# Performance work log

Hardware: AMD Instinct MI355X
Metric: run time of the kernel (lower is better)

Reference implementation:

```python
import jax, jax.numpy as jnp
import numpy as np

Dm = 512      # d_model
DI = 1024     # d_inner = 2*d_model (expand=2)
DR = 32       # dt_rank = ceil(d_model/16)
DC = 4        # d_conv
T = 3
Bb, Sf, H, W = 2, 15, 16, 11


def _ln(x, g, b):
    m = jnp.mean(x, axis=-1, keepdims=True)
    v = jnp.var(x, axis=-1, keepdims=True)
    return (x - m) * jax.lax.rsqrt(v + 1e-5) * g + b


def _mamba(x, in_w, conv_w, conv_b, xproj_w, dtproj_w, dtproj_b, A_log, D_param, out_w):
    # x: (B, L, Dm). Standard Mamba block with d_state=1.
    B, L, _ = x.shape
    xz = x @ in_w.T                                  # (B, L, 2*DI)
    xi, z = jnp.split(xz, 2, axis=-1)                # each (B, L, DI)
    # causal depthwise conv1d, kernel DC
    xc = jnp.transpose(xi, (0, 2, 1))                # (B, DI, L)
    xc = jax.lax.conv_general_dilated(
        xc, conv_w[:, None, :], (1,), [(DC - 1, 0)],
        dimension_numbers=('NCH', 'OIH', 'NCH'), feature_group_count=DI)
    xc = xc + conv_b[None, :, None]
    xi = jax.nn.silu(jnp.transpose(xc, (0, 2, 1)))   # (B, L, DI)
    x_dbl = xi @ xproj_w.T                           # (B, L, DR + 2)  (d_state=1)
    dt = x_dbl[..., :DR]
    Bc = x_dbl[..., DR:DR + 1]                       # (B, L, 1)
    Cc = x_dbl[..., DR + 1:DR + 2]                   # (B, L, 1)
    dt = jax.nn.softplus(dt @ dtproj_w.T + dtproj_b)  # (B, L, DI)
    A = -jnp.exp(A_log[:, 0])                        # (DI,), d_state=1
    dA = jnp.exp(dt * A)                             # (B, L, DI)
    dBx = dt * Bc * xi                               # (B, L, DI)
    # linear recurrence h_t = dA_t * h_{t-1} + dBx_t via parallel scan
    def comb(l, r):
        return (l[0] * r[0], r[0] * l[1] + r[1])
    _, h = jax.lax.associative_scan(comb, (dA, dBx), axis=1)
    y = Cc * h + D_param * xi                        # (B, L, DI)
    y = y * jax.nn.silu(z)
    return y @ out_w.T                               # (B, L, Dm)


def setup_inputs() -> dict:
    key = jax.random.key(0)
    ks = jax.random.split(key, 10)
    p = {}
    p['x'] = jax.random.normal(ks[0], (Bb, Sf, H, W, Dm), jnp.float32)
    p['ln1_g'] = jnp.ones((Dm,), jnp.float32)
    p['ln1_b'] = jnp.zeros((Dm,), jnp.float32)
    p['ln2_g'] = jnp.ones((Dm,), jnp.float32)
    p['ln2_b'] = jnp.zeros((Dm,), jnp.float32)
    p['mlp_w1'] = jax.random.normal(ks[1], (4 * Dm, Dm), jnp.float32) * 0.02
    p['mlp_b1'] = jnp.zeros((4 * Dm,), jnp.float32)
    p['mlp_w2'] = jax.random.normal(ks[2], (Dm, 4 * Dm), jnp.float32) * 0.02
    p['mlp_b2'] = jnp.zeros((Dm,), jnp.float32)
    p['in_w'] = jax.random.normal(ks[3], (2 * DI, Dm), jnp.float32) * 0.02
    p['conv_w'] = jax.random.normal(ks[4], (DI, DC), jnp.float32) * 0.1
    p['conv_b'] = jnp.zeros((DI,), jnp.float32)
    p['xproj_w'] = jax.random.normal(ks[5], (DR + 2, DI), jnp.float32) * 0.02
    p['dtproj_w'] = jax.random.normal(ks[6], (DI, DR), jnp.float32) * 0.1
    p['dtproj_b'] = jax.random.normal(ks[7], (DI,), jnp.float32) * 0.1
    p['A_log'] = jnp.zeros((DI, 1), jnp.float32)     # A = -1 per channel (mamba init, d_state=1)
    p['D_param'] = jnp.ones((DI,), jnp.float32)
    p['out_w'] = jax.random.normal(ks[8], (Dm, DI), jnp.float32) * 0.02
    return p


def reference(x, ln1_g, ln1_b, ln2_g, ln2_b, mlp_w1, mlp_b1, mlp_w2, mlp_b2,
              in_w, conv_w, conv_b, xproj_w, dtproj_w, dtproj_b, A_log, D_param, out_w):
    b, S, h, w, c = x.shape
    s = S // T
    xr = x.reshape(b * s, T, h, w, c)
    Bm, L = b * s, T * h * w
    # ---- part1: 4-directional mamba over flattened/flipped sequences ----
    xn = _ln(xr, ln1_g, ln1_b)
    x1 = xn.reshape(Bm, L, c)                                  # b (s h w) c
    x3 = jnp.transpose(xn, (0, 1, 3, 2, 4)).reshape(Bm, L, c)  # b (s w h) c
    cat = jnp.concatenate([x1, jnp.flip(x1, 1), x3, jnp.flip(x3, 1)], axis=0)
    y = _mamba(cat, in_w, conv_w, conv_b, xproj_w, dtproj_w, dtproj_b, A_log, D_param, out_w)
    y1, y2, y3, y4 = jnp.split(y, 4, axis=0)
    x12 = (y1 + jnp.flip(y2, 1)).reshape(Bm, T, h, w, c)
    x34 = jnp.transpose((y3 + jnp.flip(y4, 1)).reshape(Bm, T, w, h, c), (0, 1, 3, 2, 4))
    xr = xr + x12 + x34   # dropout (eval) = identity
    # ---- part2: MLP ----
    hmid = jax.nn.gelu(_ln(xr, ln2_g, ln2_b) @ mlp_w1.T + mlp_b1, approximate=False)
    xr = xr + (hmid @ mlp_w2.T + mlp_b2)
    return xr.reshape(b, S, h, w, c)
```

## Files before the change

### kernel.cpp

```cpp
#include <hip/hip_runtime.h>
#include <math.h>

typedef __attribute__((ext_vector_type(8))) short short8;
typedef __attribute__((ext_vector_type(8))) __bf16 bf16x8;
typedef __attribute__((ext_vector_type(4))) float f32x4;
typedef unsigned short ushort_t;

#define DEV __device__ __forceinline__

constexpr int Dm   = 512;
constexpr int DI   = 1024;
constexpr int DR   = 32;
constexpr int Hh   = 16;
constexpr int Wd   = 11;
constexpr int Bm   = 10;
constexpr int Lq   = 528;
constexpr int NTOK = Bm * Lq;
constexpr int MBAT = 4 * Bm;
constexpr int MTOK = MBAT * Lq;
constexpr int XD_LD = 40;
constexpr int NCHK = 16;
constexpr int CHK  = Lq / NCHK;
constexpr int MPAD = 5376;

DEV ushort_t f2bf(float f) {
    unsigned u = __float_as_uint(f);
    u += 0x7fffu + ((u >> 16) & 1u);
    return (ushort_t)(u >> 16);
}
DEV float bf2f(ushort_t h) { return __uint_as_float(((unsigned)h) << 16); }

DEV bf16x8 as_bf(short8 v) { return __builtin_bit_cast(bf16x8, v); }

DEV void mfma_bf16(f32x4& d, short8 a, short8 b) {
    d = __builtin_amdgcn_mfma_f32_16x16x32_bf16(as_bf(a), as_bf(b), d, 0, 0, 0);
}

DEV void gll16(const ushort_t* g, ushort_t* l) {
    __builtin_amdgcn_global_load_lds((const __attribute__((address_space(1))) void*)g,
                                     (__attribute__((address_space(3))) void*)l,
                                     16, 0, 0);
}

DEV float fast_erf(float x) {
    const float ax = fabsf(x);
    const float t  = 1.0f / (1.0f + 0.3275911f * ax);
    const float y  = t * (0.254829592f + t * (-0.284496736f + t * (1.421413741f
                   + t * (-1.453152027f + t * 1.061405429f))));
    const float r  = 1.0f - y * __expf(-ax * ax);
    return copysignf(r, x);
}

DEV int path_tok(int p, int bi, int q) {
    int ql = (p & 1) ? (Lq - 1 - q) : q;
    int l1;
    if (p < 2) {
        l1 = ql;
    } else {
        int t   = ql / (Hh * Wd);
        int rem = ql - t * (Hh * Wd);
        int ww  = rem / Hh;
        int hh  = rem - ww * Hh;
        l1 = (t * Hh + hh) * Wd + ww;
    }
    return bi * Lq + l1;
}

__global__ void k_f2bf(const float* __restrict__ s, ushort_t* __restrict__ d, int n) {
    int i = blockIdx.x * 256 + threadIdx.x;
    if (i < n) d[i] = f2bf(s[i]);
}
__global__ void k_zero(ushort_t* __restrict__ d, int n) {
    int i = blockIdx.x * 256 + threadIdx.x;
    if (i < n) d[i] = 0;
}
__global__ void k_cwT(const float* __restrict__ cw, float* __restrict__ cwT) {
    int i = blockIdx.x * 256 + threadIdx.x;
    if (i < 4 * DI) {
        int d = i / DI, ch = i - d * DI;
        cwT[i] = cw[ch * 4 + d];
    }
}

__global__ void k_ln1(const float* __restrict__ x, const float* __restrict__ g,
                      const float* __restrict__ b, ushort_t* __restrict__ xn) {
    const int tok  = blockIdx.x;
    const int lane = threadIdx.x;
    const int c0   = lane * 8;
    const float* row = x + (size_t)tok * Dm;
    float4 v0 = *(const float4*)(row + c0);
    float4 v1 = *(const float4*)(row + c0 + 4);
    float s  = v0.x + v0.y + v0.z + v0.w + v1.x + v1.y + v1.z + v1.w;
    float ss = v0.x*v0.x + v0.y*v0.y + v0.z*v0.z + v0.w*v0.w
             + v1.x*v1.x + v1.y*v1.y + v1.z*v1.z + v1.w*v1.w;
#pragma unroll
    for (int o = 32; o >= 1; o >>= 1) { s += __shfl_xor(s, o); ss += __shfl_xor(ss, o); }
    const float mean = s * (1.0f / Dm);
    const float rstd = rsqrtf(ss * (1.0f / Dm) - mean * mean + 1e-5f);
    float4 g0 = *(const float4*)(g + c0), g1 = *(const float4*)(g + c0 + 4);
    float4 b0 = *(const float4*)(b + c0), b1 = *(const float4*)(b + c0 + 4);
    union { uint4 u; ushort_t h[8]; } pk;
    pk.h[0] = f2bf((v0.x - mean) * rstd * g0.x + b0.x);
    pk.h[1] = f2bf((v0.y - mean) * rstd * g0.y + b0.y);
    pk.h[2] = f2bf((v0.z - mean) * rstd * g0.z + b0.z);
    pk.h[3] = f2bf((v0.w - mean) * rstd * g0.w + b0.w);
    pk.h[4] = f2bf((v1.x - mean) * rstd * g1.x + b1.x);
    pk.h[5] = f2bf((v1.y - mean) * rstd * g1.y + b1.y);
    pk.h[6] = f2bf((v1.z - mean) * rstd * g1.z + b1.z);
    pk.h[7] = f2bf((v1.w - mean) * rstd * g1.w + b1.w);
    *(uint4*)(xn + (size_t)tok * Dm + c0) = pk.u;
}

template<int BM, int BN, int EPI>
__launch_bounds__(512)
__global__ void k_gemm8w(const ushort_t* __restrict__ A, const ushort_t* __restrict__ B,
                         void* __restrict__ C, int M, int K,
                         int lda, int ldb, int ldc, int nst,
                         const float* __restrict__ bias, const float* __restrict__ resid) {
    constexpr int FM = BM / 32;
    constexpr int FN = BN / 64;
    constexpr int AP = BM / 64;
    constexpr int BP = BN / 64;
    __shared__ __align__(16) ushort_t As[2][BM * 64];
    __shared__ __align__(16) ushort_t Bs[2][BN * 64];
    const int tid  = threadIdx.x;
    const int lane = tid & 63;
    const int w    = tid >> 6;
    const int wm   = w >> 2, wn = w & 3;
    const int lr   = lane & 15, lg = lane >> 4;
    const int m0   = blockIdx.x * BM, n0 = blockIdx.y * BN;

    f32x4 acc[FM][FN] = {};

    auto stage = [&](int buf, int kb) {
#pragma unroll
        for (int i = 0; i < AP; ++i) {
            const int chunk = i * 512 + tid;
            const int r    = chunk >> 3;
            const int ccol = chunk & 7;
            const int csrc = ccol ^ (r & 7);
            gll16(A + (size_t)(m0 + r) * lda + kb + csrc * 8, As[buf] + chunk * 8);
        }
#pragma unroll
        for (int i = 0; i < BP; ++i) {
            const int chunk = i * 512 + tid;
            const int r    = chunk >> 3;
            const int ccol = chunk & 7;
            const int csrc = ccol ^ (r & 7);
            gll16(B + (size_t)(n0 + r) * ldb + kb + csrc * 8, Bs[buf] + chunk * 8);
        }
    };

    auto compute = [&](int buf) {
#pragma unroll
        for (int kk = 0; kk < 2; ++kk) {
            short8 a[FM], b[FN];
#pragma unroll
            for (int mf = 0; mf < FM; ++mf) {
                const int row = wm * (BM / 2) + mf * 16 + lr;
                const int pc  = (kk * 4 + lg) ^ (row & 7);
                a[mf] = *(const short8*)(As[buf] + (size_t)row * 64 + pc * 8);
            }
#pragma unroll
            for (int nf = 0; nf < FN; ++nf) {
                const int row = wn * (BN / 4) + nf * 16 + lr;
                const int pc  = (kk * 4 + lg) ^ (row & 7);
                b[nf] = *(const short8*)(Bs[buf] + (size_t)row * 64 + pc * 8);
            }
#pragma unroll
            for (int mf = 0; mf < FM; ++mf)
#pragma unroll
                for (int nf = 0; nf < FN; ++nf)
                    mfma_bf16(acc[mf][nf], a[mf], b[nf]);
        }
    };

    stage(0, 0);
    __syncthreads();
    int cur = 0;
    for (int kb = 64; kb < K; kb += 64) {
        stage(cur ^ 1, kb);
        compute(cur);
        __syncthreads();
        cur ^= 1;
    }
    compute(cur);

#pragma unroll
    for (int mf = 0; mf < FM; ++mf)
#pragma unroll
        for (int nf = 0; nf < FN; ++nf) {
            const int gc = n0 + wn * (BN / 4) + nf * 16 + lr;
            if (gc >= nst) continue;
#pragma unroll
            for (int r = 0; r < 4; ++r) {
                const int gm = m0 + wm * (BM / 2) + mf * 16 + lg * 4 + r;
                if (gm >= M) continue;
                float v = acc[mf][nf][r];
                const size_t oi = (size_t)gm * ldc + gc;
                if constexpr (EPI == 0) {
                    ((ushort_t*)C)[oi] = f2bf(v);
                } else if constexpr (EPI == 2) {
                    v += bias[gc];
                    v = 0.5f * v * (1.0f + fast_erf(v * 0.70710678118654752f));
                    ((ushort_t*)C)[oi] = f2bf(v);
                } else if constexpr (EPI == 3) {
                    v += bias[gc] + resid[oi];
                    ((float*)C)[oi] = v;
                } else if constexpr (EPI == 4) {
                    v += resid[oi];
                    ((float*)C)[oi] = v;
                }
            }
        }
}

template<int EPI>
__launch_bounds__(256)
__global__ void k_gemm_bt(const ushort_t* __restrict__ A, const ushort_t* __restrict__ B,
                          void* __restrict__ C, int M, int N, int K,
                          int lda, int ldb, int ldc,
                          const float* __restrict__ bias) {
    constexpr int BM = 64, BN = 64, BK = 64, LDL = BK + 8;
    __shared__ __align__(16) ushort_t As[BM][LDL];
    __shared__ __align__(16) ushort_t Bs[BN][LDL];
    const int tid  = threadIdx.x;
    const int m0   = blockIdx.x * BM, n0 = blockIdx.y * BN;
    const int lane = tid & 63;
    const int wv   = tid >> 6;
    const int wm   = wv >> 1, wn = wv & 1;
    const int lr   = lane & 15, lg = lane >> 4;

    f32x4 acc[2][2] = {};

    for (int kb = 0; kb < K; kb += BK) {
#pragma unroll
        for (int j = 0; j < 2; ++j) {
            const int chunk = tid + j * 256;
            const int row = chunk >> 3;
            const int k0  = (chunk & 7) << 3;
            const int gk  = kb + k0;
            short8 va = {};
            const int gm = m0 + row;
            if (gm < M && gk < K) va = *(const short8*)(A + (size_t)gm * lda + gk);
            *(short8*)(&As[row][k0]) = va;
            short8 vb = {};
            const int gn = n0 + row;
            if (gn < N && gk < K) vb = *(const short8*)(B + (size_t)gn * ldb + gk);
            *(short8*)(&Bs[row][k0]) = vb;
        }
        __syncthreads();
#pragma unroll
        for (int kk = 0; kk < 2; ++kk) {
            short8 a0 = *(const short8*)(&As[wm * 32 +  0 + lr][kk * 32 + lg * 8]);
            short8 a1 = *(const short8*)(&As[wm * 32 + 16 + lr][kk * 32 + lg * 8]);
            short8 b0 = *(const short8*)(&Bs[wn * 32 +  0 + lr][kk * 32 + lg * 8]);
            short8 b1 = *(const short8*)(&Bs[wn * 32 + 16 + lr][kk * 32 + lg * 8]);
            mfma_bf16(acc[0][0], a0, b0);
            mfma_bf16(acc[0][1], a0, b1);
            mfma_bf16(acc[1][0], a1, b0);
            mfma_bf16(acc[1][1], a1, b1);
        }
        __syncthreads();
    }

#pragma unroll
    for (int mf = 0; mf < 2; ++mf)
#pragma unroll
        for (int nf = 0; nf < 2; ++nf) {
            const int gc = n0 + wn * 32 + nf * 16 + lr;
            if (gc >= N) continue;
#pragma unroll
            for (int r = 0; r < 4; ++r) {
                const int gm = m0 + wm * 32 + mf * 16 + lg * 4 + r;
                if (gm >= M) continue;
                float v = acc[mf][nf][r];
                const size_t oi = (size_t)gm * ldc + gc;
                if constexpr (EPI == 0) {
                    ((ushort_t*)C)[oi] = f2bf(v);
                } else {
                    v += bias[gc];
                    v = fmaxf(v, 0.0f) + __logf(1.0f + __expf(-fabsf(v)));
                    ((ushort_t*)C)[oi] = f2bf(v);
                }
            }
        }
}

__global__ void k_conv(const ushort_t* __restrict__ xz0, const float* __restrict__ cwT,
                       const float* __restrict__ cb, ushort_t* __restrict__ xi) {
    const int idx = blockIdx.x * 256 + threadIdx.x;
    if (idx >= MTOK * 128) return;
    const int g  = idx & 127;
    const int c0 = g * 8;
    const int l  = (idx >> 7) % Lq;
    const int s  = idx / (128 * Lq);
    const int p  = s / Bm, bi = s % Bm;
    float a[8];
    {
        float4 b0 = *(const float4*)(cb + c0);
        float4 b1 = *(const float4*)(cb + c0 + 4);
        a[0]=b0.x; a[1]=b0.y; a[2]=b0.z; a[3]=b0.w;
        a[4]=b1.x; a[5]=b1.y; a[6]=b1.z; a[7]=b1.w;
    }
#pragma unroll
    for (int d = 0; d < 4; ++d) {
        const int lq = l - (3 - d);
        if (lq < 0) continue;
        const int tok = path_tok(p, bi, lq);
        union U { uint4 u; ushort_t h[8]; } xv;
        xv.u = *(const uint4*)(xz0 + (size_t)tok * (2 * DI) + c0);
        const float4 w0 = *(const float4*)(cwT + d * DI + c0);
        const float4 w1 = *(const float4*)(cwT + d * DI + c0 + 4);
        a[0] += bf2f(xv.h[0]) * w0.x;
        a[1] += bf2f(xv.h[1]) * w0.y;
        a[2] += bf2f(xv.h[2]) * w0.z;
        a[3] += bf2f(xv.h[3]) * w0.w;
        a[4] += bf2f(xv.h[4]) * w1.x;
        a[5] += bf2f(xv.h[5]) * w1.y;
        a[6] += bf2f(xv.h[6]) * w1.z;
        a[7] += bf2f(xv.h[7]) * w1.w;
    }
    union U { uint4 u; ushort_t h[8]; } ov;
#pragma unroll
    for (int k = 0; k < 8; ++k) {
        const float sv = a[k] / (1.0f + __expf(-a[k]));
        ov.h[k] = f2bf(sv);
    }
    *(uint4*)(xi + (size_t)(s * Lq + l) * DI + c0) = ov.u;
}

__global__ void k_scan1(const ushort_t* __restrict__ dt, const ushort_t* __restrict__ xz0,
                        const ushort_t* __restrict__ xdbl, const float* __restrict__ A_log,
                        const float* __restrict__ Dp, ushort_t* __restrict__ xiy,
                        ushort_t* __restrict__ corr, float* __restrict__ Pb,
                        float* __restrict__ Sb) {
    const int blk = blockIdx.x;
    const int cg = blk & 15;
    const int j  = (blk >> 4) & (NCHK - 1);
    const int s  = blk >> 8;
    const int ch = (cg << 6) + threadIdx.x;
    const int p  = s / Bm, bi = s % Bm;
    const int gl0 = j * CHK;
    const float Av = -__expf(A_log[ch]);
    const float Dv = Dp[ch];
    const size_t tok0 = (size_t)s * Lq + (size_t)gl0;
    const ushort_t* pdt = dt  + tok0 * DI + ch;
    ushort_t*       pxi = xiy + tok0 * DI + ch;
    ushort_t*       pco = corr + tok0 * DI + ch;
    const ushort_t* pbc = xdbl + tok0 * XD_LD;

    float h = 0.0f, pp = 1.0f;
    float dtv = bf2f(pdt[0]);
    float xiv = bf2f(pxi[0]);
    float zv  = bf2f(xz0[(size_t)path_tok(p, bi, gl0) * (2 * DI) + DI + ch]);
    float bc  = bf2f(pbc[32]);
    float cc  = bf2f(pbc[33]);
    for (int l = 0; l < CHK; ++l) {
        float ndt = 0.f, nxi = 0.f, nz = 0.f, nbc = 0.f, ncc = 0.f;
        if (l + 1 < CHK) {
            const size_t o = (size_t)(l + 1);
            ndt = bf2f(pdt[o * DI]);
            nxi = bf2f(pxi[o * DI]);
            nz  = bf2f(xz0[(size_t)path_tok(p, bi, gl0 + l + 1) * (2 * DI) + DI + ch]);
            nbc = bf2f(pbc[o * XD_LD + 32]);
            ncc = bf2f(pbc[o * XD_LD + 33]);
        }
        const float dA = __expf(dtv * Av);
        h = dA * h + dtv * bc * xiv;
        pp *= dA;
        const float sz = zv / (1.0f + __expf(-zv));
        pxi[(size_t)l * DI] = f2bf((cc * h + Dv * xiv) * sz);
        pco[(size_t)l * DI] = f2bf(cc * pp * sz);
        dtv = ndt; xiv = nxi; zv = nz; bc = nbc; cc = ncc;
    }
    const size_t pi = (size_t)(s * NCHK + j) * DI + ch;
    Pb[pi] = pp;
    Sb[pi] = h;
}

__global__ void k_scan2(const float* __restrict__ Pb, const float* __restrict__ Sb,
                        float* __restrict__ cb) {
    const int s  = blockIdx.x >> 4;
    const int ch = ((blockIdx.x & 15) << 6) + threadIdx.x;
    float c = 0.0f;
#pragma unroll
    for (int j = 0; j < NCHK; ++j) {
        const size_t pi = (size_t)(s * NCHK + j) * DI + ch;
        cb[pi] = c;
        c = Pb[pi] * c + Sb[pi];
    }
}

__global__ void k_ysum(const ushort_t* __restrict__ y, const ushort_t* __restrict__ corr,
                       const float* __restrict__ cbuf, ushort_t* __restrict__ ys) {
    const int tok = blockIdx.x;
    const int c0  = threadIdx.x * 8;
    const int bi = tok / Lq;
    const int l1 = tok % Lq;
    const int t  = l1 / (Hh * Wd);
    const int hw = l1 % (Hh * Wd);
    const int hh = hw / Wd, ww = hw % Wd;
    const int l3 = (t * Wd + ww) * Hh + hh;
    const int q[4] = { l1, Lq - 1 - l1, l3, Lq - 1 - l3 };
    float a[8] = {};
#pragma unroll
    for (int p = 0; p < 4; ++p) {
        const int sq = p * Bm + bi;
        const size_t off = ((size_t)sq * Lq + q[p]) * DI + c0;
        union U { uint4 u; ushort_t h[8]; } yv, cv;
        yv.u = *(const uint4*)(y + off);
        cv.u = *(const uint4*)(corr + off);
        const int j = q[p] / CHK;
        const float* cp = cbuf + ((size_t)sq * NCHK + j) * DI + c0;
        float4 ca = *(const float4*)(cp);
        float4 cb2 = *(const float4*)(cp + 4);
        a[0] += bf2f(yv.h[0]) + ca.x  * bf2f(cv.h[0]);
        a[1] += bf2f(yv.h[1]) + ca.y  * bf2f(cv.h[1]);
        a[2] += bf2f(yv.h[2]) + ca.z  * bf2f(cv.h[2]);
        a[3] += bf2f(yv.h[3]) + ca.w  * bf2f(cv.h[3]);
        a[4] += bf2f(yv.h[4]) + cb2.x * bf2f(cv.h[4]);
        a[5] += bf2f(yv.h[5]) + cb2.y * bf2f(cv.h[5]);
        a[6] += bf2f(yv.h[6]) + cb2.z * bf2f(cv.h[6]);
        a[7] += bf2f(yv.h[7]) + cb2.w * bf2f(cv.h[7]);
    }
    union U { uint4 u; ushort_t h[8]; } ov;
#pragma unroll
    for (int k = 0; k < 8; ++k) ov.h[k] = f2bf(a[k]);
    *(uint4*)(ys + (size_t)tok * DI + c0) = ov.u;
}

__global__ void k_ln2(const float* __restrict__ xin, const float* __restrict__ g,
                      const float* __restrict__ b, ushort_t* __restrict__ out) {
    const int tok  = blockIdx.x;
    const int lane = threadIdx.x;
    const int c0   = lane * 8;
    const float* row = xin + (size_t)tok * Dm;
    float4 v0 = *(const float4*)(row + c0);
    float4 v1 = *(const float4*)(row + c0 + 4);
    float s  = v0.x + v0.y + v0.z + v0.w + v1.x + v1.y + v1.z + v1.w;
    float ss = v0.x*v0.x + v0.y*v0.y + v0.z*v0.z + v0.w*v0.w
             + v1.x*v1.x + v1.y*v1.y + v1.z*v1.z + v1.w*v1.w;
#pragma unroll
    for (int o = 32; o >= 1; o >>= 1) { s += __shfl_xor(s, o); ss += __shfl_xor(ss, o); }
    const float mean = s * (1.0f / Dm);
    const float rstd = rsqrtf(ss * (1.0f / Dm) - mean * mean + 1e-5f);
    float4 g0 = *(const float4*)(g + c0), g1 = *(const float4*)(g + c0 + 4);
    float4 b0 = *(const float4*)(b + c0), b1 = *(const float4*)(b + c0 + 4);
    union { uint4 u; ushort_t h[8]; } pk;
    pk.h[0] = f2bf((v0.x - mean) * rstd * g0.x + b0.x);
    pk.h[1] = f2bf((v0.y - mean) * rstd * g0.y + b0.y);
    pk.h[2] = f2bf((v0.z - mean) * rstd * g0.z + b0.z);
    pk.h[3] = f2bf((v0.w - mean) * rstd * g0.w + b0.w);
    pk.h[4] = f2bf((v1.x - mean) * rstd * g1.x + b1.x);
    pk.h[5] = f2bf((v1.y - mean) * rstd * g1.y + b1.y);
    pk.h[6] = f2bf((v1.z - mean) * rstd * g1.z + b1.z);
    pk.h[7] = f2bf((v1.w - mean) * rstd * g1.w + b1.w);
    *(uint4*)(out + (size_t)tok * Dm + c0) = pk.u;
}

constexpr size_t OFF_CAT = 0;
constexpr size_t SZ_CAT  = (size_t)MPAD * Dm * 2;
constexpr size_t OFF_XZ0 = OFF_CAT + SZ_CAT;
constexpr size_t SZ_XZ0  = (size_t)MPAD * 2 * DI * 2;
constexpr size_t OFF_XI  = OFF_XZ0 + SZ_XZ0;
constexpr size_t SZ_XI   = (size_t)MTOK * DI * 2;
constexpr size_t OFF_XD  = OFF_XI + SZ_XI;
constexpr size_t SZ_XD   = (size_t)MTOK * XD_LD * 2;
constexpr size_t OFF_DT  = OFF_XD + SZ_XD;
constexpr size_t SZ_DT   = (size_t)MTOK * DI * 2;
constexpr size_t OFF_CO  = OFF_DT + SZ_DT;
constexpr size_t SZ_CO   = (size_t)MTOK * DI * 2;
constexpr size_t SZ_PSC  = (size_t)MBAT * NCHK * DI * 4;
constexpr size_t OFF_P   = OFF_CO + SZ_CO;
constexpr size_t OFF_S   = OFF_P + SZ_PSC;
constexpr size_t OFF_C   = OFF_S + SZ_PSC;
constexpr size_t OFF_YS  = OFF_C + SZ_PSC;
constexpr size_t SZ_YS   = (size_t)MPAD * DI * 2;
constexpr size_t OFF_XR2 = OFF_YS + SZ_YS;
constexpr size_t SZ_XR2  = (size_t)NTOK * Dm * 4;
constexpr size_t OFF_XL2 = OFF_XR2 + SZ_XR2;
constexpr size_t SZ_XL2  = (size_t)MPAD * Dm * 2;
constexpr size_t OFF_HM  = OFF_XL2 + SZ_XL2;
constexpr size_t SZ_HM   = (size_t)MPAD * 4 * Dm * 2;
constexpr size_t OFF_WIN = OFF_HM + SZ_HM;
constexpr size_t OFF_WOUT= OFF_WIN  + (size_t)2 * DI * Dm * 2;
constexpr size_t OFF_W1  = OFF_WOUT + (size_t)Dm * DI * 2;
constexpr size_t OFF_W2  = OFF_W1   + (size_t)4 * Dm * Dm * 2;
constexpr size_t OFF_WXP = OFF_W2   + (size_t)Dm * 4 * Dm * 2;
constexpr size_t OFF_WDT = OFF_WXP  + (size_t)64 * DI * 2;
constexpr size_t OFF_CWT = OFF_WDT  + (size_t)DI * DR * 2;
constexpr size_t WS_NEED = OFF_CWT  + (size_t)4 * DI * 4;

extern "C" void kernel_launch(void* const* d_in, const int* in_sizes, int n_in,
                              void* d_out, int out_size, void* d_ws, size_t ws_size,
                              hipStream_t stream) {
    const float* x        = (const float*)d_in[0];
    const float* ln1_g    = (const float*)d_in[1];
    const float* ln1_b    = (const float*)d_in[2];
    const float* ln2_g    = (const float*)d_in[3];
    const float* ln2_b    = (const float*)d_in[4];
    const float* mlp_w1   = (const float*)d_in[5];
    const float* mlp_b1   = (const float*)d_in[6];
    const float* mlp_w2   = (const float*)d_in[7];
    const float* mlp_b2   = (const float*)d_in[8];
    const float* in_w     = (const float*)d_in[9];
    const float* conv_w   = (const float*)d_in[10];
    const float* conv_b   = (const float*)d_in[11];
    const float* xproj_w  = (const float*)d_in[12];
    const float* dtproj_w = (const float*)d_in[13];
    const float* dtproj_b = (const float*)d_in[14];
    const float* A_log    = (const float*)d_in[15];
    const float* D_param  = (const float*)d_in[16];
    const float* out_w    = (const float*)d_in[17];

    if (ws_size < WS_NEED) return;

    char* ws = (char*)d_ws;
    ushort_t* cat   = (ushort_t*)(ws + OFF_CAT);
    ushort_t* xz0   = (ushort_t*)(ws + OFF_XZ0);
    ushort_t* xi    = (ushort_t*)(ws + OFF_XI);
    ushort_t* xdbl  = (ushort_t*)(ws + OFF_XD);
    ushort_t* dtb   = (ushort_t*)(ws + OFF_DT);
    ushort_t* corr  = (ushort_t*)(ws + OFF_CO);
    float*    Pb    = (float*)   (ws + OFF_P);
    float*    Sb    = (float*)   (ws + OFF_S);
    float*    cb    = (float*)   (ws + OFF_C);
    ushort_t* ysum  = (ushort_t*)(ws + OFF_YS);
    float*    xr2   = (float*)   (ws + OFF_XR2);
    ushort_t* xln2  = (ushort_t*)(ws + OFF_XL2);
    ushort_t* hmid  = (ushort_t*)(ws + OFF_HM);
    ushort_t* w_in  = (ushort_t*)(ws + OFF_WIN);
    ushort_t* w_out = (ushort_t*)(ws + OFF_WOUT);
    ushort_t* w_1   = (ushort_t*)(ws + OFF_W1);
    ushort_t* w_2   = (ushort_t*)(ws + OFF_W2);
    ushort_t* w_xp  = (ushort_t*)(ws + OFF_WXP);
    ushort_t* w_dt  = (ushort_t*)(ws + OFF_WDT);
    float*    cwT   = (float*)   (ws + OFF_CWT);

    auto cvt = [&](const float* s, ushort_t* d, int n) {
        k_f2bf<<<(n + 255) / 256, 256, 0, stream>>>(s, d, n);
    };
    cvt(in_w,     w_in,  2 * DI * Dm);
    cvt(out_w,    w_out, Dm * DI);
    cvt(mlp_w1,   w_1,   4 * Dm * Dm);
    cvt(mlp_w2,   w_2,   Dm * 4 * Dm);
    k_zero<<<(64 * DI + 255) / 256, 256, 0, stream>>>(w_xp, 64 * DI);
    cvt(xproj_w,  w_xp,  (DR + 2) * DI);
    cvt(dtproj_w, w_dt,  DI * DR);
    k_cwT<<<(4 * DI + 255) / 256, 256, 0, stream>>>(conv_w, cwT);

    k_ln1<<<NTOK, 64, 0, stream>>>(x, ln1_g, ln1_b, cat);

    k_gemm8w<64, 128, 0><<<dim3(MPAD / 64, (2 * DI) / 128), 512, 0, stream>>>(
        cat, w_in, xz0, NTOK, Dm, Dm, Dm, 2 * DI, 2 * DI, nullptr, nullptr);

    k_conv<<<(MTOK * 128 + 255) / 256, 256, 0, stream>>>(xz0, cwT, conv_b, xi);

    k_gemm8w<64, 64, 0><<<dim3(MTOK / 64, 1), 512, 0, stream>>>(
        xi, w_xp, xdbl, MTOK, DI, DI, DI, XD_LD, DR + 2, nullptr, nullptr);

    k_gemm_bt<1><<<dim3(MTOK / 64, DI / 64), 256, 0, stream>>>(
        xdbl, w_dt, dtb, MTOK, DI, DR, XD_LD, DR, DI, dtproj_b);

    k_scan1<<<MBAT * NCHK * 16, 64, 0, stream>>>(dtb, xz0, xdbl, A_log, D_param,
                                                 xi, corr, Pb, Sb);
    k_scan2<<<MBAT * 16, 64, 0, stream>>>(Pb, Sb, cb);

    k_ysum<<<NTOK, 128, 0, stream>>>(xi, corr, cb, ysum);

    k_gemm8w<64, 128, 4><<<dim3(MPAD / 64, Dm / 128), 512, 0, stream>>>(
        ysum, w_out, xr2, NTOK, DI, DI, DI, Dm, Dm, nullptr, x);

    k_ln2<<<NTOK, 64, 0, stream>>>(xr2, ln2_g, ln2_b, xln2);

    k_gemm8w<64, 128, 2><<<dim3(MPAD / 64, (4 * Dm) / 128), 512, 0, stream>>>(
        xln2, w_1, hmid, NTOK, Dm, Dm, Dm, 4 * Dm, 4 * Dm, mlp_b1, nullptr);

    k_gemm8w<64, 128, 3><<<dim3(MPAD / 64, Dm / 128), 512, 0, stream>>>(
        hmid, w_2, (float*)d_out, NTOK, 4 * Dm, 4 * Dm, 4 * Dm, Dm, Dm, mlp_b2, xr2);
}
```

Measured before the change: 261.1 us.

## Move silu(z) gating from scan into ysum and reuse 8-wave GEMM for dt_proj

Removes the per-timestep gathered z loads and silu from the scan kernel. The gate is now applied once per token in k_ysum, reading z contiguously from xz0. This relies on the gate factoring out of the four direction sums, since they all refer to the same token's z. The dt projection now runs on the pipelined k_gemm8w template instead of the simpler k_gemm_bt, with the x_dbl stride and dt weights padded to K=64 (zero-filled) so the template's K tiling fits, at the cost of some wasted MFMA work on the zero padding.

```diff
diff --git a/kernel.cpp b/kernel.cpp
--- a/kernel.cpp
+++ b/kernel.cpp
@@ -18,7 +18,7 @@
 constexpr int NTOK = Bm * Lq;
 constexpr int MBAT = 4 * Bm;
 constexpr int MTOK = MBAT * Lq;
-constexpr int XD_LD = 40;
+constexpr int XD_LD = 64;
 constexpr int NCHK = 16;
 constexpr int CHK  = Lq / NCHK;
 constexpr int MPAD = 5376;
@@ -79,6 +79,13 @@
     if (i < 4 * DI) {
         int d = i / DI, ch = i - d * DI;
         cwT[i] = cw[ch * 4 + d];
+    }
+}
+__global__ void k_cvt_dt(const float* __restrict__ s, ushort_t* __restrict__ d) {
+    int i = blockIdx.x * 256 + threadIdx.x;
+    if (i < DI * DR) {
+        int r = i / DR, c = i - r * DR;
+        d[r * 64 + c] = f2bf(s[i]);
     }
 }
 
@@ -200,6 +207,10 @@
                 const size_t oi = (size_t)gm * ldc + gc;
                 if constexpr (EPI == 0) {
                     ((ushort_t*)C)[oi] = f2bf(v);
+                } else if constexpr (EPI == 1) {
+                    v += bias[gc];
+                    v = fmaxf(v, 0.0f) + __logf(1.0f + __expf(-fabsf(v)));
+                    ((ushort_t*)C)[oi] = f2bf(v);
                 } else if constexpr (EPI == 2) {
                     v += bias[gc];
                     v = 0.5f * v * (1.0f + fast_erf(v * 0.70710678118654752f));
@@ -210,78 +221,6 @@
                 } else if constexpr (EPI == 4) {
                     v += resid[oi];
                     ((float*)C)[oi] = v;
-                }
-            }
-        }
-}
-
-template<int EPI>
-__launch_bounds__(256)
-__global__ void k_gemm_bt(const ushort_t* __restrict__ A, const ushort_t* __restrict__ B,
-                          void* __restrict__ C, int M, int N, int K,
-                          int lda, int ldb, int ldc,
-                          const float* __restrict__ bias) {
-    constexpr int BM = 64, BN = 64, BK = 64, LDL = BK + 8;
-    __shared__ __align__(16) ushort_t As[BM][LDL];
-    __shared__ __align__(16) ushort_t Bs[BN][LDL];
-    const int tid  = threadIdx.x;
-    const int m0   = blockIdx.x * BM, n0 = blockIdx.y * BN;
-    const int lane = tid & 63;
-    const int wv   = tid >> 6;
-    const int wm   = wv >> 1, wn = wv & 1;
-    const int lr   = lane & 15, lg = lane >> 4;
-
-    f32x4 acc[2][2] = {};
-
-    for (int kb = 0; kb < K; kb += BK) {
-#pragma unroll
-        for (int j = 0; j < 2; ++j) {
-            const int chunk = tid + j * 256;
-            const int row = chunk >> 3;
-            const int k0  = (chunk & 7) << 3;
-            const int gk  = kb + k0;
-            short8 va = {};
-            const int gm = m0 + row;
-            if (gm < M && gk < K) va = *(const short8*)(A + (size_t)gm * lda + gk);
-            *(short8*)(&As[row][k0]) = va;
-            short8 vb = {};
-            const int gn = n0 + row;
-            if (gn < N && gk < K) vb = *(const short8*)(B + (size_t)gn * ldb + gk);
-            *(short8*)(&Bs[row][k0]) = vb;
-        }
-        __syncthreads();
-#pragma unroll
-        for (int kk = 0; kk < 2; ++kk) {
-            short8 a0 = *(const short8*)(&As[wm * 32 +  0 + lr][kk * 32 + lg * 8]);
-            short8 a1 = *(const short8*)(&As[wm * 32 + 16 + lr][kk * 32 + lg * 8]);
-            short8 b0 = *(const short8*)(&Bs[wn * 32 +  0 + lr][kk * 32 + lg * 8]);
-            short8 b1 = *(const short8*)(&Bs[wn * 32 + 16 + lr][kk * 32 + lg * 8]);
-            mfma_bf16(acc[0][0], a0, b0);
-            mfma_bf16(acc[0][1], a0, b1);
-            mfma_bf16(acc[1][0], a1, b0);
-            mfma_bf16(acc[1][1], a1, b1);
-        }
-        __syncthreads();
-    }
-
-#pragma unroll
-    for (int mf = 0; mf < 2; ++mf)
-#pragma unroll
-        for (int nf = 0; nf < 2; ++nf) {
-            const int gc = n0 + wn * 32 + nf * 16 + lr;
-            if (gc >= N) continue;
-#pragma unroll
-            for (int r = 0; r < 4; ++r) {
-                const int gm = m0 + wm * 32 + mf * 16 + lg * 4 + r;
-                if (gm >= M) continue;
-                float v = acc[mf][nf][r];
-                const size_t oi = (size_t)gm * ldc + gc;
-                if constexpr (EPI == 0) {
-                    ((ushort_t*)C)[oi] = f2bf(v);
-                } else {
-                    v += bias[gc];
-                    v = fmaxf(v, 0.0f) + __logf(1.0f + __expf(-fabsf(v)));
-                    ((ushort_t*)C)[oi] = f2bf(v);
                 }
             }
         }
@@ -330,7 +269,7 @@
     *(uint4*)(xi + (size_t)(s * Lq + l) * DI + c0) = ov.u;
 }
 
-__global__ void k_scan1(const ushort_t* __restrict__ dt, const ushort_t* __restrict__ xz0,
+__global__ void k_scan1(const ushort_t* __restrict__ dt,
                         const ushort_t* __restrict__ xdbl, const float* __restrict__ A_log,
                         const float* __restrict__ Dp, ushort_t* __restrict__ xiy,
                         ushort_t* __restrict__ corr, float* __restrict__ Pb,
@@ -340,7 +279,6 @@
     const int j  = (blk >> 4) & (NCHK - 1);
     const int s  = blk >> 8;
     const int ch = (cg << 6) + threadIdx.x;
-    const int p  = s / Bm, bi = s % Bm;
     const int gl0 = j * CHK;
     const float Av = -__expf(A_log[ch]);
     const float Dv = Dp[ch];
@@ -353,26 +291,23 @@
     float h = 0.0f, pp = 1.0f;
     float dtv = bf2f(pdt[0]);
     float xiv = bf2f(pxi[0]);
-    float zv  = bf2f(xz0[(size_t)path_tok(p, bi, gl0) * (2 * DI) + DI + ch]);
     float bc  = bf2f(pbc[32]);
     float cc  = bf2f(pbc[33]);
     for (int l = 0; l < CHK; ++l) {
-        float ndt = 0.f, nxi = 0.f, nz = 0.f, nbc = 0.f, ncc = 0.f;
+        float ndt = 0.f, nxi = 0.f, nbc = 0.f, ncc = 0.f;
         if (l + 1 < CHK) {
             const size_t o = (size_t)(l + 1);
             ndt = bf2f(pdt[o * DI]);
             nxi = bf2f(pxi[o * DI]);
-            nz  = bf2f(xz0[(size_t)path_tok(p, bi, gl0 + l + 1) * (2 * DI) + DI + ch]);
             nbc = bf2f(pbc[o * XD_LD + 32]);
             ncc = bf2f(pbc[o * XD_LD + 33]);
         }
         const float dA = __expf(dtv * Av);
         h = dA * h + dtv * bc * xiv;
         pp *= dA;
-        const float sz = zv / (1.0f + __expf(-zv));
-        pxi[(size_t)l * DI] = f2bf((cc * h + Dv * xiv) * sz);
-        pco[(size_t)l * DI] = f2bf(cc * pp * sz);
-        dtv = ndt; xiv = nxi; zv = nz; bc = nbc; cc = ncc;
+        pxi[(size_t)l * DI] = f2bf(cc * h + Dv * xiv);
+        pco[(size_t)l * DI] = f2bf(cc * pp);
+        dtv = ndt; xiv = nxi; bc = nbc; cc = ncc;
     }
     const size_t pi = (size_t)(s * NCHK + j) * DI + ch;
     Pb[pi] = pp;
@@ -393,7 +328,8 @@
 }
 
 __global__ void k_ysum(const ushort_t* __restrict__ y, const ushort_t* __restrict__ corr,
-                       const float* __restrict__ cbuf, ushort_t* __restrict__ ys) {
+                       const float* __restrict__ cbuf, const ushort_t* __restrict__ xz0,
+                       ushort_t* __restrict__ ys) {
     const int tok = blockIdx.x;
     const int c0  = threadIdx.x * 8;
     const int bi = tok / Lq;
@@ -424,9 +360,14 @@
         a[6] += bf2f(yv.h[6]) + cb2.z * bf2f(cv.h[6]);
         a[7] += bf2f(yv.h[7]) + cb2.w * bf2f(cv.h[7]);
     }
+    union Z { uint4 u; ushort_t h[8]; } zv;
+    zv.u = *(const uint4*)(xz0 + (size_t)tok * (2 * DI) + DI + c0);
     union U { uint4 u; ushort_t h[8]; } ov;
 #pragma unroll
-    for (int k = 0; k < 8; ++k) ov.h[k] = f2bf(a[k]);
+    for (int k = 0; k < 8; ++k) {
+        const float z = bf2f(zv.h[k]);
+        ov.h[k] = f2bf(a[k] * z / (1.0f + __expf(-z)));
+    }
     *(uint4*)(ys + (size_t)tok * DI + c0) = ov.u;
 }
 
@@ -489,7 +430,7 @@
 constexpr size_t OFF_W2  = OFF_W1   + (size_t)4 * Dm * Dm * 2;
 constexpr size_t OFF_WXP = OFF_W2   + (size_t)Dm * 4 * Dm * 2;
 constexpr size_t OFF_WDT = OFF_WXP  + (size_t)64 * DI * 2;
-constexpr size_t OFF_CWT = OFF_WDT  + (size_t)DI * DR * 2;
+constexpr size_t OFF_CWT = OFF_WDT  + (size_t)DI * 64 * 2;
 constexpr size_t WS_NEED = OFF_CWT  + (size_t)4 * DI * 4;
 
 extern "C" void kernel_launch(void* const* d_in, const int* in_sizes, int n_in,
@@ -547,7 +488,8 @@
     cvt(mlp_w2,   w_2,   Dm * 4 * Dm);
     k_zero<<<(64 * DI + 255) / 256, 256, 0, stream>>>(w_xp, 64 * DI);
     cvt(xproj_w,  w_xp,  (DR + 2) * DI);
-    cvt(dtproj_w, w_dt,  DI * DR);
+    k_zero<<<(DI * 64 + 255) / 256, 256, 0, stream>>>(w_dt, DI * 64);
+    k_cvt_dt<<<(DI * DR + 255) / 256, 256, 0, stream>>>(dtproj_w, w_dt);
     k_cwT<<<(4 * DI + 255) / 256, 256, 0, stream>>>(conv_w, cwT);
 
     k_ln1<<<NTOK, 64, 0, stream>>>(x, ln1_g, ln1_b, cat);
@@ -558,16 +500,16 @@
     k_conv<<<(MTOK * 128 + 255) / 256, 256, 0, stream>>>(xz0, cwT, conv_b, xi);
 
     k_gemm8w<64, 64, 0><<<dim3(MTOK / 64, 1), 512, 0, stream>>>(
-        xi, w_xp, xdbl, MTOK, DI, DI, DI, XD_LD, DR + 2, nullptr, nullptr);
-
-    k_gemm_bt<1><<<dim3(MTOK / 64, DI / 64), 256, 0, stream>>>(
-        xdbl, w_dt, dtb, MTOK, DI, DR, XD_LD, DR, DI, dtproj_b);
-
-    k_scan1<<<MBAT * NCHK * 16, 64, 0, stream>>>(dtb, xz0, xdbl, A_log, D_param,
+        xi, w_xp, xdbl, MTOK, DI, DI, DI, XD_LD, 64, nullptr, nullptr);
+
+    k_gemm8w<64, 128, 1><<<dim3(MTOK / 64, DI / 128), 512, 0, stream>>>(
+        xdbl, w_dt, dtb, MTOK, 64, XD_LD, 64, DI, DI, dtproj_b, nullptr);
+
+    k_scan1<<<MBAT * NCHK * 16, 64, 0, stream>>>(dtb, xdbl, A_log, D_param,
                                                  xi, corr, Pb, Sb);
     k_scan2<<<MBAT * 16, 64, 0, stream>>>(Pb, Sb, cb);
 
-    k_ysum<<<NTOK, 128, 0, stream>>>(xi, corr, cb, ysum);
+    k_ysum<<<NTOK, 128, 0, stream>>>(xi, corr, cb, xz0, ysum);
 
     k_gemm8w<64, 128, 4><<<dim3(MPAD / 64, Dm / 128), 512, 0, stream>>>(
         ysum, w_out, xr2, NTOK, DI, DI, DI, Dm, Dm, nullptr, x);
```

Result: no change. 258.6 us (-1.0%).
